# Kernel tuning notes

Measured on AMD Instinct MI355X. Metric: run time of the kernel, lower is better.

## Reference

```python
import jax, jax.numpy as jnp
import numpy as np

SIZE = 11
SIGMA = 1.5
K1, K2, L = 0.01, 0.03, 1.0
C1 = (K1 * L) ** 2
C2 = (K2 * L) ** 2


def _fspecial_gauss(size=SIZE, sigma=SIGMA):
    # mimic MATLAB fspecial('gaussian'): grid -5..5 for size=11
    x, y = np.mgrid[-size // 2 + 1:size // 2 + 1, -size // 2 + 1:size // 2 + 1]
    g = np.exp(-((x.astype(np.float32) ** 2 + y.astype(np.float32) ** 2) / (2.0 * sigma ** 2)))
    g = g / g.sum()
    return jnp.asarray(g, dtype=jnp.float32)[None, None]  # [1,1,11,11] OIHW


def _conv_valid(x, w):
    # x: [B,1,H,W], w: [1,1,k,k], stride 1, no padding
    return jax.lax.conv_general_dilated(
        x, w, window_strides=(1, 1), padding='VALID',
        dimension_numbers=('NCHW', 'OIHW', 'NCHW'))


def setup_inputs() -> dict:
    key = jax.random.key(0)
    k1, k2 = jax.random.split(key)
    sr_image = jax.random.uniform(k1, (16, 3, 512, 512), dtype=jnp.float32)
    hr_image = jax.random.uniform(k2, (16, 3, 512, 512), dtype=jnp.float32)
    return {"sr_image": sr_image, "hr_image": hr_image}


def reference(sr_image, hr_image):
    hr = hr_image[:, 0:1, :, :]
    sr = sr_image[:, 0:1, :, :]
    window = _fspecial_gauss()
    mu1 = _conv_valid(hr, window)
    mu2 = _conv_valid(sr, window)
    mu1_sq = mu1 * mu1
    mu2_sq = mu2 * mu2
    mu1_mu2 = mu1 * mu2
    sigma1_sq = _conv_valid(hr * hr, window) - mu1_sq
    sigma2_sq = _conv_valid(sr * sr, window) - mu2_sq
    sigma12 = _conv_valid(hr * sr, window) - mu1_mu2
    value = ((2 * mu1_mu2 + C1) * (2 * sigma12 + C2)
             / ((mu1_sq + mu2_sq + C1) * (sigma1_sq + sigma2_sq + C2)))
    return jnp.mean(value)
```

## Files before the change

kernel.cpp:

```cpp
#include <hip/hip_runtime.h>

#define TW 32
#define TH 48
#define HR 58
#define IMG_W 512
#define OUT_W 502
#define CH_STRIDE (3 * IMG_W * IMG_W)
#define GX 16
#define GY 11
#define GZ 16
#define NBLK (GX * GY * GZ)

typedef float f2 __attribute__((ext_vector_type(2)));

__global__ __launch_bounds__(256, 4) void ssim_main_kernel(
    const float* __restrict__ sr_img,
    const float* __restrict__ hr_img,
    float* __restrict__ partial)
{
    __shared__ __align__(16) f2    M12[HR][TW + 2];
    __shared__ __align__(16) f2    SQ [HR][TW + 2];
    __shared__ __align__(16) float XY [HR][TW + 4];
    __shared__ float red[4];

    const int t  = threadIdx.x;
    const int x0 = blockIdx.x * TW;
    const int y0 = blockIdx.y * TH;
    const int b  = blockIdx.z;

    const float Wf[11] = {
        0.00102838f, 0.00759876f, 0.03600077f, 0.10936069f, 0.21300554f,
        0.26601173f,
        0.21300554f, 0.10936069f, 0.03600077f, 0.00759876f, 0.00102838f
    };
    const f2 W2[11] = {
        {0.00102838f,0.00102838f}, {0.00759876f,0.00759876f},
        {0.03600077f,0.03600077f}, {0.10936069f,0.10936069f},
        {0.21300554f,0.21300554f}, {0.26601173f,0.26601173f},
        {0.21300554f,0.21300554f}, {0.10936069f,0.10936069f},
        {0.03600077f,0.03600077f}, {0.00759876f,0.00759876f},
        {0.00102838f,0.00102838f}
    };

    const float* __restrict__ hrp = hr_img + (size_t)b * CH_STRIDE;
    const float* __restrict__ srp = sr_img + (size_t)b * CH_STRIDE;

    if (t < 4 * HR) {
        int r  = t >> 2;
        int c0 = (t & 3) * 8;
        int gy = y0 + r; if (gy > IMG_W - 1) gy = IMG_W - 1;
        const float4* hrow = (const float4*)(hrp + (size_t)gy * IMG_W + x0 + c0);
        const float4* srow = (const float4*)(srp + (size_t)gy * IMG_W + x0 + c0);

        f2 hs[20];
#pragma unroll
        for (int q = 0; q < 5; ++q) {
            float4 va = hrow[q];
            float4 vb = srow[q];
            hs[4*q+0] = (f2){va.x, vb.x};
            hs[4*q+1] = (f2){va.y, vb.y};
            hs[4*q+2] = (f2){va.z, vb.z};
            hs[4*q+3] = (f2){va.w, vb.w};
        }

        f2 a12[8], asq[8];
        float axy[8];
#pragma unroll
        for (int j = 0; j < 8; ++j) {
            a12[j] = (f2){0.f, 0.f};
            asq[j] = (f2){0.f, 0.f};
            axy[j] = 0.f;
        }
#pragma unroll
        for (int k = 0; k < 11; ++k) {
            f2 wp = W2[k];
            float wk = Wf[k];
#pragma unroll
            for (int j = 0; j < 8; ++j) {
                f2 x = hs[j + k];
                a12[j] += wp * x;
                asq[j] += wp * (x * x);
                axy[j]  = fmaf(wk, x.x * x.y, axy[j]);
            }
        }
        *(float4*)&M12[r][c0+0] = make_float4(a12[0].x,a12[0].y,a12[1].x,a12[1].y);
        *(float4*)&M12[r][c0+2] = make_float4(a12[2].x,a12[2].y,a12[3].x,a12[3].y);
        *(float4*)&M12[r][c0+4] = make_float4(a12[4].x,a12[4].y,a12[5].x,a12[5].y);
        *(float4*)&M12[r][c0+6] = make_float4(a12[6].x,a12[6].y,a12[7].x,a12[7].y);
        *(float4*)&SQ [r][c0+0] = make_float4(asq[0].x,asq[0].y,asq[1].x,asq[1].y);
        *(float4*)&SQ [r][c0+2] = make_float4(asq[2].x,asq[2].y,asq[3].x,asq[3].y);
        *(float4*)&SQ [r][c0+4] = make_float4(asq[4].x,asq[4].y,asq[5].x,asq[5].y);
        *(float4*)&SQ [r][c0+6] = make_float4(asq[6].x,asq[6].y,asq[7].x,asq[7].y);
        *(float4*)&XY [r][c0+0] = make_float4(axy[0],axy[1],axy[2],axy[3]);
        *(float4*)&XY [r][c0+4] = make_float4(axy[4],axy[5],axy[6],axy[7]);
    }
    __syncthreads();

    const float C1v = 1e-4f, C2v = 9e-4f;
    float local = 0.f;
    {
        int c  = t & 31;
        int r0 = (t >> 5) * 6;

        f2 am[6], as_[6];
        float ax[6];
#pragma unroll
        for (int j = 0; j < 6; ++j) {
            am[j] = (f2){0.f, 0.f};
            as_[j] = (f2){0.f, 0.f};
            ax[j] = 0.f;
        }

#pragma unroll
        for (int i = 0; i < 16; ++i) {
            f2 vm = M12[r0 + i][c];
            f2 vs = SQ [r0 + i][c];
            float vx = XY[r0 + i][c];
#pragma unroll
            for (int j = 0; j < 6; ++j) {
                int k = i - j;
                if (k >= 0 && k <= 10) {
                    am[j]  += W2[k] * vm;
                    as_[j] += W2[k] * vs;
                    ax[j]   = fmaf(Wf[k], vx, ax[j]);
                }
            }
        }

        int ox = x0 + c;
#pragma unroll
        for (int j = 0; j < 6; ++j) {
            int oy = y0 + r0 + j;
            if (oy < OUT_W && ox < OUT_W) {
                float m1 = am[j].x, m2 = am[j].y;
                float mu1s = m1 * m1, mu2s = m2 * m2, m12 = m1 * m2;
                float s1 = as_[j].x - mu1s, s2 = as_[j].y - mu2s, s12 = ax[j] - m12;
                float num = (2.f * m12 + C1v) * (2.f * s12 + C2v);
                float den = (mu1s + mu2s + C1v) * (s1 + s2 + C2v);
                local += num / den;
            }
        }
    }

#pragma unroll
    for (int off = 32; off > 0; off >>= 1)
        local += __shfl_down(local, off);
    if ((t & 63) == 0) red[t >> 6] = local;
    __syncthreads();
    if (t == 0) {
        int blk = (blockIdx.z * GY + blockIdx.y) * GX + blockIdx.x;
        partial[blk] = red[0] + red[1] + red[2] + red[3];
    }
}

__global__ __launch_bounds__(256) void ssim_finalize(
    const float* __restrict__ partial, float* __restrict__ out)
{
    __shared__ float red[4];
    int t = threadIdx.x;
    float s = 0.f;
#pragma unroll
    for (int i = 0; i < NBLK / 256; ++i)
        s += partial[t + i * 256];
#pragma unroll
    for (int off = 32; off > 0; off >>= 1)
        s += __shfl_down(s, off);
    if ((t & 63) == 0) red[t >> 6] = s;
    __syncthreads();
    if (t == 0)
        out[0] = (red[0] + red[1] + red[2] + red[3]) * (1.0f / (16.0f * 502.0f * 502.0f));
}

extern "C" void kernel_launch(void* const* d_in, const int* in_sizes, int n_in,
                              void* d_out, int out_size, void* d_ws, size_t ws_size,
                              hipStream_t stream)
{
    const float* sr = (const float*)d_in[0];
    const float* hr = (const float*)d_in[1];
    float* out = (float*)d_out;
    float* partial = (float*)d_ws;

    dim3 grid(GX, GY, GZ);
    ssim_main_kernel<<<grid, 256, 0, stream>>>(sr, hr, partial);
    ssim_finalize<<<1, 256, 0, stream>>>(partial, out);
}
```

Baseline: 119.3 us.

## Fuse finalize into main kernel via atomic ticket and repack shared layout

The separate finalize launch is removed. Each block now bumps an atomic ticket, and the last block to finish reduces the partial sums and writes the mean. The shared memory layout interleaves the mean and square sums into one padded float4 array, so the vertical pass does a single 128-bit LDS read per row. The horizontal pass is reordered to iterate over input pixels, computing squares once per pixel instead of once per tap. A hipMemsetAsync is added each call, and the fence plus atomic adds a small serial tail at the end of every block.

```diff
diff --git a/kernel.cpp b/kernel.cpp
--- a/kernel.cpp
+++ b/kernel.cpp
@@ -10,17 +10,21 @@
 #define GY 11
 #define GZ 16
 #define NBLK (GX * GY * GZ)
+#define MSQS 35
+#define XYS  36
 
 typedef float f2 __attribute__((ext_vector_type(2)));
+typedef float f4 __attribute__((ext_vector_type(4)));
 
 __global__ __launch_bounds__(256, 4) void ssim_main_kernel(
     const float* __restrict__ sr_img,
     const float* __restrict__ hr_img,
-    float* __restrict__ partial)
+    float* __restrict__ partial,
+    unsigned int* __restrict__ ticket,
+    float* __restrict__ out)
 {
-    __shared__ __align__(16) f2    M12[HR][TW + 2];
-    __shared__ __align__(16) f2    SQ [HR][TW + 2];
-    __shared__ __align__(16) float XY [HR][TW + 4];
+    __shared__ f4    MSQ[HR][MSQS];
+    __shared__ float XY [HR][XYS];
     __shared__ float red[4];
 
     const int t  = threadIdx.x;
@@ -72,27 +76,27 @@
             axy[j] = 0.f;
         }
 #pragma unroll
-        for (int k = 0; k < 11; ++k) {
-            f2 wp = W2[k];
-            float wk = Wf[k];
+        for (int p = 0; p < 18; ++p) {
+            f2 xp  = hs[p];
+            f2 xp2 = xp * xp;
+            float xyp = xp.x * xp.y;
 #pragma unroll
             for (int j = 0; j < 8; ++j) {
-                f2 x = hs[j + k];
-                a12[j] += wp * x;
-                asq[j] += wp * (x * x);
-                axy[j]  = fmaf(wk, x.x * x.y, axy[j]);
+                int k = p - j;
+                if (k >= 0 && k <= 10) {
+                    a12[j] += W2[k] * xp;
+                    asq[j] += W2[k] * xp2;
+                    axy[j]  = fmaf(Wf[k], xyp, axy[j]);
+                }
             }
         }
-        *(float4*)&M12[r][c0+0] = make_float4(a12[0].x,a12[0].y,a12[1].x,a12[1].y);
-        *(float4*)&M12[r][c0+2] = make_float4(a12[2].x,a12[2].y,a12[3].x,a12[3].y);
-        *(float4*)&M12[r][c0+4] = make_float4(a12[4].x,a12[4].y,a12[5].x,a12[5].y);
-        *(float4*)&M12[r][c0+6] = make_float4(a12[6].x,a12[6].y,a12[7].x,a12[7].y);
-        *(float4*)&SQ [r][c0+0] = make_float4(asq[0].x,asq[0].y,asq[1].x,asq[1].y);
-        *(float4*)&SQ [r][c0+2] = make_float4(asq[2].x,asq[2].y,asq[3].x,asq[3].y);
-        *(float4*)&SQ [r][c0+4] = make_float4(asq[4].x,asq[4].y,asq[5].x,asq[5].y);
-        *(float4*)&SQ [r][c0+6] = make_float4(asq[6].x,asq[6].y,asq[7].x,asq[7].y);
-        *(float4*)&XY [r][c0+0] = make_float4(axy[0],axy[1],axy[2],axy[3]);
-        *(float4*)&XY [r][c0+4] = make_float4(axy[4],axy[5],axy[6],axy[7]);
+
+        int cb = c0 + (c0 >> 3);
+#pragma unroll
+        for (int u = 0; u < 8; ++u)
+            MSQ[r][cb + u] = (f4){a12[u].x, a12[u].y, asq[u].x, asq[u].y};
+        *(float4*)&XY[r][c0]   = make_float4(axy[0],axy[1],axy[2],axy[3]);
+        *(float4*)&XY[r][c0+4] = make_float4(axy[4],axy[5],axy[6],axy[7]);
     }
     __syncthreads();
 
@@ -101,27 +105,29 @@
     {
         int c  = t & 31;
         int r0 = (t >> 5) * 6;
+        int cs = c + (c >> 3);
 
-        f2 am[6], as_[6];
+        f2 am[6], as2[6];
         float ax[6];
 #pragma unroll
         for (int j = 0; j < 6; ++j) {
             am[j] = (f2){0.f, 0.f};
-            as_[j] = (f2){0.f, 0.f};
+            as2[j] = (f2){0.f, 0.f};
             ax[j] = 0.f;
         }
 
 #pragma unroll
         for (int i = 0; i < 16; ++i) {
-            f2 vm = M12[r0 + i][c];
-            f2 vs = SQ [r0 + i][c];
+            f4 v = MSQ[r0 + i][cs];
             float vx = XY[r0 + i][c];
+            f2 vm = (f2){v.x, v.y};
+            f2 vs = (f2){v.z, v.w};
 #pragma unroll
             for (int j = 0; j < 6; ++j) {
                 int k = i - j;
                 if (k >= 0 && k <= 10) {
                     am[j]  += W2[k] * vm;
-                    as_[j] += W2[k] * vs;
+                    as2[j] += W2[k] * vs;
                     ax[j]   = fmaf(Wf[k], vx, ax[j]);
                 }
             }
@@ -134,7 +140,7 @@
             if (oy < OUT_W && ox < OUT_W) {
                 float m1 = am[j].x, m2 = am[j].y;
                 float mu1s = m1 * m1, mu2s = m2 * m2, m12 = m1 * m2;
-                float s1 = as_[j].x - mu1s, s2 = as_[j].y - mu2s, s12 = ax[j] - m12;
+                float s1 = as2[j].x - mu1s, s2 = as2[j].y - mu2s, s12 = ax[j] - m12;
                 float num = (2.f * m12 + C1v) * (2.f * s12 + C2v);
                 float den = (mu1s + mu2s + C1v) * (s1 + s2 + C2v);
                 local += num / den;
@@ -147,28 +153,32 @@
         local += __shfl_down(local, off);
     if ((t & 63) == 0) red[t >> 6] = local;
     __syncthreads();
+
+    const int blk = (blockIdx.z * GY + blockIdx.y) * GX + blockIdx.x;
     if (t == 0) {
-        int blk = (blockIdx.z * GY + blockIdx.y) * GX + blockIdx.x;
         partial[blk] = red[0] + red[1] + red[2] + red[3];
+        __threadfence();
+        unsigned old = atomicAdd(ticket, 1u);
+        red[0] = (old == NBLK - 1) ? 1.f : 0.f;
     }
-}
+    __syncthreads();
+    bool last = (red[0] != 0.f);
+    __syncthreads();
 
-__global__ __launch_bounds__(256) void ssim_finalize(
-    const float* __restrict__ partial, float* __restrict__ out)
-{
-    __shared__ float red[4];
-    int t = threadIdx.x;
-    float s = 0.f;
+    if (last) {
+        __threadfence();
+        float s = 0.f;
 #pragma unroll
-    for (int i = 0; i < NBLK / 256; ++i)
-        s += partial[t + i * 256];
+        for (int i = 0; i < NBLK / 256; ++i)
+            s += partial[t + i * 256];
 #pragma unroll
-    for (int off = 32; off > 0; off >>= 1)
-        s += __shfl_down(s, off);
-    if ((t & 63) == 0) red[t >> 6] = s;
-    __syncthreads();
-    if (t == 0)
-        out[0] = (red[0] + red[1] + red[2] + red[3]) * (1.0f / (16.0f * 502.0f * 502.0f));
+        for (int off = 32; off > 0; off >>= 1)
+            s += __shfl_down(s, off);
+        if ((t & 63) == 0) red[t >> 6] = s;
+        __syncthreads();
+        if (t == 0)
+            out[0] = (red[0] + red[1] + red[2] + red[3]) * (1.0f / (16.0f * 502.0f * 502.0f));
+    }
 }
 
 extern "C" void kernel_launch(void* const* d_in, const int* in_sizes, int n_in,
@@ -179,8 +189,9 @@
     const float* hr = (const float*)d_in[1];
     float* out = (float*)d_out;
     float* partial = (float*)d_ws;
+    unsigned int* ticket = (unsigned int*)((char*)d_ws + 16384);
 
+    hipMemsetAsync(ticket, 0, 4, stream);
     dim3 grid(GX, GY, GZ);
-    ssim_main_kernel<<<grid, 256, 0, stream>>>(sr, hr, partial);
-    ssim_finalize<<<1, 256, 0, stream>>>(partial, out);
+    ssim_main_kernel<<<grid, 256, 0, stream>>>(sr, hr, partial, ticket, out);
 }
```

New measurement: 183.5 us. 53.7% more time.
